# Performance work log

Measured on AMD Instinct MI355X. Metric: run time of the kernel, lower is better.

## Reference

```python
import jax, jax.numpy as jnp
import numpy as np

B, S, D, H = 2, 2048, 1024, 16
HD = D // H            # head_dim = 64
CHUNK = 1024           # hard-coded in the torch module
ROPE_THETA = 10000.0


def setup_inputs() -> dict:
    key = jax.random.key(0)
    ks = jax.random.split(key, 5)
    hidden_states = jax.random.normal(ks[0], (B, S, D), dtype=jnp.float32)
    # Precomputed RoPE frequencies: freqs_cis[s, j] = exp(i * s * theta_j),
    # stored as real [S, HD//2, 2] = (cos, sin).
    inv_freq = 1.0 / (ROPE_THETA ** (np.arange(0, HD, 2, dtype=np.float32) / HD))
    ang = np.outer(np.arange(S, dtype=np.float32), inv_freq)  # [S, HD//2]
    freqs_cis = jnp.stack([jnp.cos(ang), jnp.sin(ang)], axis=-1).astype(jnp.float32)
    scale = 0.02
    Wq = jax.random.normal(ks[1], (D, D), dtype=jnp.float32) * scale
    Wk = jax.random.normal(ks[2], (D, D), dtype=jnp.float32) * scale
    Wv = jax.random.normal(ks[3], (D, D), dtype=jnp.float32) * scale
    Wo = jax.random.normal(ks[4], (D, D), dtype=jnp.float32) * scale
    return {"hidden_states": hidden_states, "freqs_cis": freqs_cis,
            "Wq": Wq, "Wk": Wk, "Wv": Wv, "Wo": Wo}


def _apply_rope(x, freqs_cis):
    # x: [B, S, H, HD]; freqs_cis: [S, HD//2, 2] (cos, sin)
    b, s, h, hd = x.shape
    xr = x.reshape(b, s, h, hd // 2, 2)
    a, bb = xr[..., 0], xr[..., 1]
    c = freqs_cis[:s, :, 0][None, :, None, :]  # broadcast over batch, heads
    d = freqs_cis[:s, :, 1][None, :, None, :]
    # complex multiply (a + ib)(c + id)
    out = jnp.stack([a * c - bb * d, a * d + bb * c], axis=-1)
    return out.reshape(b, s, h, hd)


def reference(hidden_states, freqs_cis, Wq, Wk, Wv, Wo):
    b, s, dm = hidden_states.shape
    q = (hidden_states @ Wq).reshape(b, s, H, HD)
    k = (hidden_states @ Wk).reshape(b, s, H, HD)
    v = (hidden_states @ Wv).reshape(b, s, H, HD)
    q = _apply_rope(q, freqs_cis)
    k = _apply_rope(k, freqs_cis)
    q = q.transpose(0, 2, 1, 3)  # [B, H, S, HD]
    k = k.transpose(0, 2, 1, 3)
    v = v.transpose(0, 2, 1, 3)
    scaling = HD ** (-0.5)
    out = jnp.zeros_like(q)
    # Faithful replication of the (buggy) chunked attention: softmax is
    # normalized PER key-chunk, then chunk outputs are summed.
    for i in range(0, s, CHUNK):
        j = min(i + CHUNK, s)
        w = jnp.einsum('bhqd,bhkd->bhqk', q, k[:, :, i:j]) * scaling
        w = jax.nn.softmax(w.astype(jnp.float32), axis=-1).astype(q.dtype)
        out = out + jnp.einsum('bhqk,bhkd->bhqd', w, v[:, :, i:j])
    out = out.transpose(0, 2, 1, 3).reshape(b, s, dm)
    return out @ Wo
```

## Files before the change

kernel.cpp:

```cpp
#include <hip/hip_runtime.h>
#include <hip/hip_bf16.h>
#include <cstdint>

typedef __bf16 bf16x8 __attribute__((ext_vector_type(8)));
typedef float f32x4 __attribute__((ext_vector_type(4)));
typedef float f32x16 __attribute__((ext_vector_type(16)));

#define MFMA16(a, b, c) __builtin_amdgcn_mfma_f32_16x16x32_bf16(a, b, c, 0, 0, 0)
#define MFMA32(a, b, c) __builtin_amdgcn_mfma_f32_32x32x16_bf16(a, b, c, 0, 0, 0)

__device__ __forceinline__ void gload_lds16(const void* g, void* l) {
  __builtin_amdgcn_global_load_lds(
      (const __attribute__((address_space(1))) unsigned int*)g,
      (__attribute__((address_space(3))) unsigned int*)l, 16, 0, 0);
}

__device__ __forceinline__ unsigned short f2bf(float x) {
  union { float f; uint32_t u; } v; v.f = x;
  uint32_t r = v.u + 0x7fff + ((v.u >> 16) & 1);
  return (unsigned short)(r >> 16);
}
__device__ __forceinline__ float bf2f(unsigned short h) {
  union { float f; uint32_t u; } v; v.u = ((uint32_t)h) << 16;
  return v.f;
}
__device__ __forceinline__ f32x16 fzero16() {
  f32x16 v;
#pragma unroll
  for (int i = 0; i < 16; ++i) v[i] = 0.f;
  return v;
}

__global__ __launch_bounds__(256) void k_split(const float* __restrict__ x,
                                               unsigned short* __restrict__ hi, int n4) {
  int i = blockIdx.x * blockDim.x + threadIdx.x;
  if (i >= n4) return;
  float4 v = ((const float4*)x)[i];
  ushort4 h;
  h.x = f2bf(v.x); h.y = f2bf(v.y); h.z = f2bf(v.z); h.w = f2bf(v.w);
  ((ushort4*)hi)[i] = h;
}

__global__ __launch_bounds__(256) void k_wsplit(
    const float* __restrict__ Wq, const float* __restrict__ Wk,
    const float* __restrict__ Wv, const float* __restrict__ Wo,
    unsigned short* __restrict__ WtqH, unsigned short* __restrict__ WtkH,
    unsigned short* __restrict__ WtvH, unsigned short* __restrict__ WtoH) {
  const int z = blockIdx.z;
  const float* W = (z == 0) ? Wq : (z == 1) ? Wk : (z == 2) ? Wv : Wo;
  unsigned short* WtH = (z == 0) ? WtqH : (z == 1) ? WtkH : (z == 2) ? WtvH : WtoH;
  __shared__ float tile[32][33];
  const int bx = blockIdx.x, by = blockIdx.y;
  const int tx = threadIdx.x & 31, ty = threadIdx.x >> 5;
#pragma unroll
  for (int i = 0; i < 4; ++i)
    tile[ty + i * 8][tx] = W[(size_t)(by * 32 + ty + i * 8) * 1024 + bx * 32 + tx];
  __syncthreads();
#pragma unroll
  for (int i = 0; i < 4; ++i) {
    float v = tile[tx][ty + i * 8];
    WtH[(size_t)(bx * 32 + ty + i * 8) * 1024 + by * 32 + tx] = f2bf(v);
  }
}

__global__ __launch_bounds__(256, 2) void k_qkv(
    const unsigned short* __restrict__ hsH,
    const unsigned short* __restrict__ WqH, const unsigned short* __restrict__ WkH,
    const unsigned short* __restrict__ WvH, const float* __restrict__ freqs,
    unsigned short* __restrict__ qB, unsigned short* __restrict__ kB,
    unsigned short* __restrict__ vB) {
  __shared__ unsigned short Ah[128 * 32], Bh[128 * 32];
  const int tid = threadIdx.x;
  const int bm = blockIdx.y, bn = blockIdx.x;
  const int w = bn >> 3;
  const int n0 = (bn & 7) * 128;
  const unsigned short* WH = (w == 0) ? WqH : (w == 1) ? WkH : WvH;
  const int lane = tid & 63, wave = tid >> 6;
  const int wm = (wave & 1) * 64, wn = (wave >> 1) * 64;
  const int l15 = lane & 15, lq = lane >> 4;

  f32x4 acc[4][4];
#pragma unroll
  for (int i = 0; i < 4; i++)
#pragma unroll
    for (int j = 0; j < 4; j++) acc[i][j] = (f32x4){0.f, 0.f, 0.f, 0.f};

  const char* baseA = (const char*)hsH + (size_t)(bm * 128) * 2048;
  const char* baseB = (const char*)WH + (size_t)n0 * 2048;
  const int off0 = tid << 4, row0 = off0 >> 6, seg0 = off0 & 63;
  const int off1 = (tid + 256) << 4, row1 = off1 >> 6, seg1 = off1 & 63;

  for (int k0 = 0; k0 < 1024; k0 += 32) {
    __syncthreads();
    gload_lds16(baseA + (size_t)row0 * 2048 + k0 * 2 + seg0, (char*)Ah + wave * 1024);
    gload_lds16(baseB + (size_t)row0 * 2048 + k0 * 2 + seg0, (char*)Bh + wave * 1024);
    gload_lds16(baseA + (size_t)row1 * 2048 + k0 * 2 + seg1,
                (char*)Ah + 4096 + wave * 1024);
    gload_lds16(baseB + (size_t)row1 * 2048 + k0 * 2 + seg1,
                (char*)Bh + 4096 + wave * 1024);
    __syncthreads();
    bf16x8 ah[4], bh[4];
#pragma unroll
    for (int i = 0; i < 4; ++i) {
      ah[i] = *(const bf16x8*)&Ah[(wm + i * 16 + l15) * 32 + lq * 8];
      bh[i] = *(const bf16x8*)&Bh[(wn + i * 16 + l15) * 32 + lq * 8];
    }
#pragma unroll
    for (int i = 0; i < 4; ++i)
#pragma unroll
      for (int j = 0; j < 4; ++j) acc[i][j] = MFMA16(ah[i], bh[j], acc[i][j]);
  }

  unsigned short* dst = (w == 0) ? qB : (w == 1) ? kB : vB;
#pragma unroll
  for (int i = 0; i < 4; ++i) {
#pragma unroll
    for (int j = 0; j < 4; ++j) {
      int colw = n0 + wn + j * 16 + l15;
      int h = colw >> 6, d = colw & 63;
#pragma unroll
      for (int r = 0; r < 4; ++r) {
        int rowg = bm * 128 + wm + i * 16 + lq * 4 + r;
        int s = rowg & 2047, b = rowg >> 11;
        float val = acc[i][j][r];
        if (w < 2) {
          float partner = __shfl_xor(val, 1);
          int jj = d >> 1;
          float cs = freqs[(s * 32 + jj) * 2 + 0];
          float sn = freqs[(s * 32 + jj) * 2 + 1];
          float res = (d & 1) ? (partner * sn + val * cs) : (val * cs - partner * sn);
          dst[(((size_t)(b * 16 + h)) * 2048 + s) * 64 + d] = f2bf(res);
        } else {
          dst[(((size_t)(b * 16 + h)) * 64 + d) * 2048 + s] = f2bf(val);
        }
      }
    }
  }
}

#define LDP 72

__global__ __launch_bounds__(256, 2) void k_attn(
    const unsigned short* __restrict__ qB, const unsigned short* __restrict__ kB,
    const unsigned short* __restrict__ vB,
    unsigned short* __restrict__ c0, unsigned short* __restrict__ c1) {
  __shared__ unsigned short Pt[4 * 64 * LDP];
  const int tid = threadIdx.x, lane = tid & 63, wave = tid >> 6;
  const int l31 = lane & 31, lh = lane >> 5;
  const int bid = blockIdx.x;
  const int x = (bid >> 3) & 7;
  const int gg = (bid & 7) + 8 * (bid >> 6);
  const int bh = gg & 31;
  const int chunk = gg >> 5;
  const int q0 = x * 256 + wave * 64;
  const size_t base = (size_t)bh * 2048 * 64;
  const float sc = 0.125f * 1.44269504089f;

  bf16x8 qf[2][4];
#pragma unroll
  for (int qt = 0; qt < 2; ++qt)
#pragma unroll
    for (int ks = 0; ks < 4; ++ks)
      qf[qt][ks] = *(const bf16x8*)(qB + base + (size_t)(q0 + qt * 32 + l31) * 64 +
                                    ks * 16 + lh * 8);

  const unsigned short* kp = kB + base + (size_t)chunk * 1024 * 64 + l31 * 64 + lh * 8;
  const unsigned short* vp = vB + base + l31 * 2048 + chunk * 1024 + lh * 8;
  unsigned short* Pw = Pt + wave * (64 * LDP);

  bf16x8 kfa[4], kfb[4];
#pragma unroll
  for (int ks = 0; ks < 4; ++ks) {
    kfa[ks] = *(const bf16x8*)(kp + ks * 16);
    kfb[ks] = *(const bf16x8*)(kp + 2048 + ks * 16);
  }
  kp += 4096;

  f32x16 o[2][2];
#pragma unroll
  for (int a = 0; a < 2; ++a)
#pragma unroll
    for (int bq = 0; bq < 2; ++bq) o[a][bq] = fzero16();
  float rsum[2] = {0.f, 0.f};

  for (int kb = 0; kb < 16; ++kb) {
    bf16x8 vf[2][4];
#pragma unroll
    for (int dt = 0; dt < 2; ++dt)
#pragma unroll
      for (int ks = 0; ks < 4; ++ks)
        vf[dt][ks] = *(const bf16x8*)(vp + dt * 65536 + ks * 16);

#pragma unroll
    for (int mt = 0; mt < 2; ++mt) {
      f32x16 s0 = fzero16(), s1 = fzero16();
      if (mt == 0) {
#pragma unroll
        for (int ks = 0; ks < 4; ++ks) {
          s0 = MFMA32(kfa[ks], qf[0][ks], s0);
          s1 = MFMA32(kfa[ks], qf[1][ks], s1);
        }
#pragma unroll
        for (int ks = 0; ks < 4; ++ks) kfa[ks] = *(const bf16x8*)(kp + ks * 16);
      } else {
#pragma unroll
        for (int ks = 0; ks < 4; ++ks) {
          s0 = MFMA32(kfb[ks], qf[0][ks], s0);
          s1 = MFMA32(kfb[ks], qf[1][ks], s1);
        }
#pragma unroll
        for (int ks = 0; ks < 4; ++ks)
          kfb[ks] = *(const bf16x8*)(kp + 2048 + ks * 16);
      }
#pragma unroll
      for (int qt = 0; qt < 2; ++qt) {
        const f32x16& sv = qt ? s1 : s0;
        float ps[16];
        float rs = 0.f;
#pragma unroll
        for (int r = 0; r < 16; ++r) {
          ps[r] = __builtin_exp2f(sv[r] * sc);
          rs += ps[r];
        }
        rsum[qt] += rs;
        unsigned int* prow =
            (unsigned int*)(Pw + (qt * 32 + l31) * LDP + mt * 32 + 4 * lh);
#pragma unroll
        for (int p = 0; p < 8; ++p) {
          union { unsigned int u; __bf16 h2[2]; } pk;
          pk.h2[0] = (__bf16)ps[2 * p];
          pk.h2[1] = (__bf16)ps[2 * p + 1];
          prow[4 * (p >> 1) + (p & 1)] = pk.u;
        }
      }
    }
    kp += 4096;

#pragma unroll
    for (int qt = 0; qt < 2; ++qt)
#pragma unroll
      for (int ks = 0; ks < 4; ++ks) {
        bf16x8 pf = *(const bf16x8*)(Pw + (qt * 32 + l31) * LDP + ks * 16 + lh * 8);
        o[0][qt] = MFMA32(vf[0][ks], pf, o[0][qt]);
        o[1][qt] = MFMA32(vf[1][ks], pf, o[1][qt]);
      }
    vp += 64;
  }

  unsigned short* cB = chunk ? c1 : c0;
  const int b = bh >> 4, h = bh & 15;
#pragma unroll
  for (int qt = 0; qt < 2; ++qt) {
    float lsum = rsum[qt] + __shfl_xor(rsum[qt], 32);
    float inv = 1.f / lsum;
    int s = q0 + qt * 32 + l31;
#pragma unroll
    for (int dt = 0; dt < 2; ++dt)
#pragma unroll
      for (int g = 0; g < 4; ++g) {
        int d = dt * 32 + 4 * lh + 8 * g;
        size_t idx = ((size_t)(b * 2048 + s)) * 1024 + h * 64 + d;
        ushort4 hv;
#pragma unroll
        for (int t = 0; t < 4; ++t)
          ((unsigned short*)&hv)[t] = f2bf(o[dt][qt][g * 4 + t] * inv);
        *(ushort4*)(cB + idx) = hv;
      }
  }
}

__global__ __launch_bounds__(256) void k_comb(const unsigned short* __restrict__ c0,
                                              const unsigned short* __restrict__ c1,
                                              unsigned short* __restrict__ outB,
                                              int n8) {
  int i = blockIdx.x * blockDim.x + threadIdx.x;
  if (i >= n8) return;
  uint4 a = ((const uint4*)c0)[i];
  uint4 b = ((const uint4*)c1)[i];
  uint4 r;
  const unsigned short* pa = (const unsigned short*)&a;
  const unsigned short* pb = (const unsigned short*)&b;
  unsigned short* pr = (unsigned short*)&r;
#pragma unroll
  for (int j = 0; j < 8; ++j) pr[j] = f2bf(bf2f(pa[j]) + bf2f(pb[j]));
  ((uint4*)outB)[i] = r;
}

__global__ __launch_bounds__(256, 2) void k_out(const unsigned short* __restrict__ A,
                                                const unsigned short* __restrict__ B,
                                                float* __restrict__ out) {
  __shared__ unsigned short Ah[128 * 32], Bh[128 * 32];
  const int tid = threadIdx.x;
  const int bm = blockIdx.y, n0 = blockIdx.x * 128;
  const int lane = tid & 63, wave = tid >> 6;
  const int wm = (wave & 1) * 64, wn = (wave >> 1) * 64;
  const int l15 = lane & 15, lq = lane >> 4;

  f32x4 acc[4][4];
#pragma unroll
  for (int i = 0; i < 4; i++)
#pragma unroll
    for (int j = 0; j < 4; j++) acc[i][j] = (f32x4){0.f, 0.f, 0.f, 0.f};

  const char* baseA = (const char*)A + (size_t)(bm * 128) * 2048;
  const char* baseB = (const char*)B + (size_t)n0 * 2048;
  const int off0 = tid << 4, row0 = off0 >> 6, seg0 = off0 & 63;
  const int off1 = (tid + 256) << 4, row1 = off1 >> 6, seg1 = off1 & 63;

  for (int k0 = 0; k0 < 1024; k0 += 32) {
    __syncthreads();
    gload_lds16(baseA + (size_t)row0 * 2048 + k0 * 2 + seg0, (char*)Ah + wave * 1024);
    gload_lds16(baseB + (size_t)row0 * 2048 + k0 * 2 + seg0, (char*)Bh + wave * 1024);
    gload_lds16(baseA + (size_t)row1 * 2048 + k0 * 2 + seg1,
                (char*)Ah + 4096 + wave * 1024);
    gload_lds16(baseB + (size_t)row1 * 2048 + k0 * 2 + seg1,
                (char*)Bh + 4096 + wave * 1024);
    __syncthreads();
    bf16x8 ah[4], bh[4];
#pragma unroll
    for (int i = 0; i < 4; ++i) {
      ah[i] = *(const bf16x8*)&Ah[(wm + i * 16 + l15) * 32 + lq * 8];
      bh[i] = *(const bf16x8*)&Bh[(wn + i * 16 + l15) * 32 + lq * 8];
    }
#pragma unroll
    for (int i = 0; i < 4; ++i)
#pragma unroll
      for (int j = 0; j < 4; ++j) acc[i][j] = MFMA16(ah[i], bh[j], acc[i][j]);
  }
#pragma unroll
  for (int i = 0; i < 4; ++i)
#pragma unroll
    for (int j = 0; j < 4; ++j) {
      int colw = n0 + wn + j * 16 + l15;
#pragma unroll
      for (int r = 0; r < 4; ++r) {
        int rowg = bm * 128 + wm + i * 16 + lq * 4 + r;
        out[(size_t)rowg * 1024 + colw] = acc[i][j][r];
      }
    }
}

extern "C" void kernel_launch(void* const* d_in, const int* in_sizes, int n_in,
                              void* d_out, int out_size, void* d_ws, size_t ws_size,
                              hipStream_t stream) {
  const float* hs = (const float*)d_in[0];
  const float* freqs = (const float*)d_in[1];
  const float* Wq = (const float*)d_in[2];
  const float* Wk = (const float*)d_in[3];
  const float* Wv = (const float*)d_in[4];
  const float* Wo = (const float*)d_in[5];
  float* out = (float*)d_out;

  const size_t MD = (size_t)4096 * 1024;
  const size_t WW = (size_t)1024 * 1024;
  unsigned short* hsH = (unsigned short*)d_ws;
  unsigned short* WtqH = hsH + MD;
  unsigned short* WtkH = WtqH + WW;
  unsigned short* WtvH = WtkH + WW;
  unsigned short* WtoH = WtvH + WW;
  unsigned short* qB = WtoH + WW;
  unsigned short* kB = qB + MD;
  unsigned short* vB = kB + MD;
  unsigned short* c0 = vB + MD;
  unsigned short* c1 = c0 + MD;
  unsigned short* attnB = hsH;

  k_split<<<4096, 256, 0, stream>>>(hs, hsH, (int)(MD / 4));
  k_wsplit<<<dim3(32, 32, 4), 256, 0, stream>>>(Wq, Wk, Wv, Wo,
                                                WtqH, WtkH, WtvH, WtoH);
  k_qkv<<<dim3(24, 32), 256, 0, stream>>>(hsH, WtqH, WtkH, WtvH, freqs, qB, kB, vB);
  k_attn<<<512, 256, 0, stream>>>(qB, kB, vB, c0, c1);
  k_comb<<<2048, 256, 0, stream>>>(c0, c1, attnB, (int)(MD / 8));
  k_out<<<dim3(8, 32), 256, 0, stream>>>(attnB, WtoH, out);
}
```

Before: 258.7 us.

## Split attention keys into four partial chunks and unroll QKV GEMM K-loop

```diff
diff --git a/kernel.cpp b/kernel.cpp
--- a/kernel.cpp
+++ b/kernel.cpp
@@ -69,7 +69,8 @@
     const unsigned short* __restrict__ WvH, const float* __restrict__ freqs,
     unsigned short* __restrict__ qB, unsigned short* __restrict__ kB,
     unsigned short* __restrict__ vB) {
-  __shared__ unsigned short Ah[128 * 32], Bh[128 * 32];
+  __shared__ unsigned short Ah0[128 * 32], Bh0[128 * 32];
+  __shared__ unsigned short Ah1[128 * 32], Bh1[128 * 32];
   const int tid = threadIdx.x;
   const int bm = blockIdx.y, bn = blockIdx.x;
   const int w = bn >> 3;
@@ -90,20 +91,37 @@
   const int off0 = tid << 4, row0 = off0 >> 6, seg0 = off0 & 63;
   const int off1 = (tid + 256) << 4, row1 = off1 >> 6, seg1 = off1 & 63;
 
-  for (int k0 = 0; k0 < 1024; k0 += 32) {
+  for (int k0 = 0; k0 < 1024; k0 += 64) {
     __syncthreads();
-    gload_lds16(baseA + (size_t)row0 * 2048 + k0 * 2 + seg0, (char*)Ah + wave * 1024);
-    gload_lds16(baseB + (size_t)row0 * 2048 + k0 * 2 + seg0, (char*)Bh + wave * 1024);
+    gload_lds16(baseA + (size_t)row0 * 2048 + k0 * 2 + seg0, (char*)Ah0 + wave * 1024);
+    gload_lds16(baseB + (size_t)row0 * 2048 + k0 * 2 + seg0, (char*)Bh0 + wave * 1024);
     gload_lds16(baseA + (size_t)row1 * 2048 + k0 * 2 + seg1,
-                (char*)Ah + 4096 + wave * 1024);
+                (char*)Ah0 + 4096 + wave * 1024);
     gload_lds16(baseB + (size_t)row1 * 2048 + k0 * 2 + seg1,
-                (char*)Bh + 4096 + wave * 1024);
+                (char*)Bh0 + 4096 + wave * 1024);
+    gload_lds16(baseA + (size_t)row0 * 2048 + (k0 + 32) * 2 + seg0,
+                (char*)Ah1 + wave * 1024);
+    gload_lds16(baseB + (size_t)row0 * 2048 + (k0 + 32) * 2 + seg0,
+                (char*)Bh1 + wave * 1024);
+    gload_lds16(baseA + (size_t)row1 * 2048 + (k0 + 32) * 2 + seg1,
+                (char*)Ah1 + 4096 + wave * 1024);
+    gload_lds16(baseB + (size_t)row1 * 2048 + (k0 + 32) * 2 + seg1,
+                (char*)Bh1 + 4096 + wave * 1024);
     __syncthreads();
     bf16x8 ah[4], bh[4];
 #pragma unroll
     for (int i = 0; i < 4; ++i) {
-      ah[i] = *(const bf16x8*)&Ah[(wm + i * 16 + l15) * 32 + lq * 8];
-      bh[i] = *(const bf16x8*)&Bh[(wn + i * 16 + l15) * 32 + lq * 8];
+      ah[i] = *(const bf16x8*)&Ah0[(wm + i * 16 + l15) * 32 + lq * 8];
+      bh[i] = *(const bf16x8*)&Bh0[(wn + i * 16 + l15) * 32 + lq * 8];
+    }
+#pragma unroll
+    for (int i = 0; i < 4; ++i)
+#pragma unroll
+      for (int j = 0; j < 4; ++j) acc[i][j] = MFMA16(ah[i], bh[j], acc[i][j]);
+#pragma unroll
+    for (int i = 0; i < 4; ++i) {
+      ah[i] = *(const bf16x8*)&Ah1[(wm + i * 16 + l15) * 32 + lq * 8];
+      bh[i] = *(const bf16x8*)&Bh1[(wn + i * 16 + l15) * 32 + lq * 8];
     }
 #pragma unroll
     for (int i = 0; i < 4; ++i)
@@ -140,10 +158,10 @@
 
 #define LDP 72
 
-__global__ __launch_bounds__(256, 2) void k_attn(
+__global__ __launch_bounds__(256, 3) void k_attn(
     const unsigned short* __restrict__ qB, const unsigned short* __restrict__ kB,
     const unsigned short* __restrict__ vB,
-    unsigned short* __restrict__ c0, unsigned short* __restrict__ c1) {
+    unsigned short* __restrict__ cP, float* __restrict__ rsW) {
   __shared__ unsigned short Pt[4 * 64 * LDP];
   const int tid = threadIdx.x, lane = tid & 63, wave = tid >> 6;
   const int l31 = lane & 31, lh = lane >> 5;
@@ -151,7 +169,8 @@
   const int x = (bid >> 3) & 7;
   const int gg = (bid & 7) + 8 * (bid >> 6);
   const int bh = gg & 31;
-  const int chunk = gg >> 5;
+  const int z = gg >> 5;
+  const int key00 = (z >> 1) * 1024 + (z & 1) * 512;
   const int q0 = x * 256 + wave * 64;
   const size_t base = (size_t)bh * 2048 * 64;
   const float sc = 0.125f * 1.44269504089f;
@@ -164,8 +183,8 @@
       qf[qt][ks] = *(const bf16x8*)(qB + base + (size_t)(q0 + qt * 32 + l31) * 64 +
                                     ks * 16 + lh * 8);
 
-  const unsigned short* kp = kB + base + (size_t)chunk * 1024 * 64 + l31 * 64 + lh * 8;
-  const unsigned short* vp = vB + base + l31 * 2048 + chunk * 1024 + lh * 8;
+  const unsigned short* kp = kB + base + (size_t)key00 * 64 + l31 * 64 + lh * 8;
+  const unsigned short* vp = vB + base + l31 * 2048 + key00 + lh * 8;
   unsigned short* Pw = Pt + wave * (64 * LDP);
 
   bf16x8 kfa[4], kfb[4];
@@ -183,7 +202,7 @@
     for (int bq = 0; bq < 2; ++bq) o[a][bq] = fzero16();
   float rsum[2] = {0.f, 0.f};
 
-  for (int kb = 0; kb < 16; ++kb) {
+  for (int kb = 0; kb < 8; ++kb) {
     bf16x8 vf[2][4];
 #pragma unroll
     for (int dt = 0; dt < 2; ++dt)
@@ -247,13 +266,13 @@
     vp += 64;
   }
 
-  unsigned short* cB = chunk ? c1 : c0;
+  unsigned short* cB = cP + (size_t)z * (4096 * 1024);
   const int b = bh >> 4, h = bh & 15;
 #pragma unroll
   for (int qt = 0; qt < 2; ++qt) {
     float lsum = rsum[qt] + __shfl_xor(rsum[qt], 32);
-    float inv = 1.f / lsum;
     int s = q0 + qt * 32 + l31;
+    if (lh == 0) rsW[((size_t)z * 32 + bh) * 2048 + s] = lsum;
 #pragma unroll
     for (int dt = 0; dt < 2; ++dt)
 #pragma unroll
@@ -263,26 +282,43 @@
         ushort4 hv;
 #pragma unroll
         for (int t = 0; t < 4; ++t)
-          ((unsigned short*)&hv)[t] = f2bf(o[dt][qt][g * 4 + t] * inv);
+          ((unsigned short*)&hv)[t] = f2bf(o[dt][qt][g * 4 + t]);
         *(ushort4*)(cB + idx) = hv;
       }
   }
 }
 
-__global__ __launch_bounds__(256) void k_comb(const unsigned short* __restrict__ c0,
-                                              const unsigned short* __restrict__ c1,
+__global__ __launch_bounds__(256) void k_comb(const unsigned short* __restrict__ cP,
+                                              const float* __restrict__ rsW,
                                               unsigned short* __restrict__ outB,
                                               int n8) {
   int i = blockIdx.x * blockDim.x + threadIdx.x;
   if (i >= n8) return;
-  uint4 a = ((const uint4*)c0)[i];
-  uint4 b = ((const uint4*)c1)[i];
+  const size_t MD = (size_t)4096 * 1024;
+  int flat = i * 8;
+  int col = flat & 1023;
+  int srow = (flat >> 10) & 2047;
+  int b = flat >> 21;
+  int bh = b * 16 + (col >> 6);
+  float l0 = rsW[(size_t)(0 * 32 + bh) * 2048 + srow] +
+             rsW[(size_t)(1 * 32 + bh) * 2048 + srow];
+  float l1 = rsW[(size_t)(2 * 32 + bh) * 2048 + srow] +
+             rsW[(size_t)(3 * 32 + bh) * 2048 + srow];
+  float i0 = 1.f / l0, i1 = 1.f / l1;
+  uint4 a0 = ((const uint4*)cP)[i];
+  uint4 a1 = ((const uint4*)(cP + MD))[i];
+  uint4 a2 = ((const uint4*)(cP + 2 * MD))[i];
+  uint4 a3 = ((const uint4*)(cP + 3 * MD))[i];
   uint4 r;
-  const unsigned short* pa = (const unsigned short*)&a;
-  const unsigned short* pb = (const unsigned short*)&b;
+  const unsigned short* p0 = (const unsigned short*)&a0;
+  const unsigned short* p1 = (const unsigned short*)&a1;
+  const unsigned short* p2 = (const unsigned short*)&a2;
+  const unsigned short* p3 = (const unsigned short*)&a3;
   unsigned short* pr = (unsigned short*)&r;
 #pragma unroll
-  for (int j = 0; j < 8; ++j) pr[j] = f2bf(bf2f(pa[j]) + bf2f(pb[j]));
+  for (int j = 0; j < 8; ++j)
+    pr[j] = f2bf((bf2f(p0[j]) + bf2f(p1[j])) * i0 +
+                 (bf2f(p2[j]) + bf2f(p3[j])) * i1);
   ((uint4*)outB)[i] = r;
 }
 
@@ -361,15 +397,15 @@
   unsigned short* qB = WtoH + WW;
   unsigned short* kB = qB + MD;
   unsigned short* vB = kB + MD;
-  unsigned short* c0 = vB + MD;
-  unsigned short* c1 = c0 + MD;
+  unsigned short* cP = vB + MD;
+  float* rsW = (float*)(cP + 4 * MD);
   unsigned short* attnB = hsH;
 
   k_split<<<4096, 256, 0, stream>>>(hs, hsH, (int)(MD / 4));
   k_wsplit<<<dim3(32, 32, 4), 256, 0, stream>>>(Wq, Wk, Wv, Wo,
                                                 WtqH, WtkH, WtvH, WtoH);
   k_qkv<<<dim3(24, 32), 256, 0, stream>>>(hsH, WtqH, WtkH, WtvH, freqs, qB, kB, vB);
-  k_attn<<<512, 256, 0, stream>>>(qB, kB, vB, c0, c1);
-  k_comb<<<2048, 256, 0, stream>>>(c0, c1, attnB, (int)(MD / 8));
+  k_attn<<<1024, 256, 0, stream>>>(qB, kB, vB, cP, rsW);
+  k_comb<<<2048, 256, 0, stream>>>(cP, rsW, attnB, (int)(MD / 8));
   k_out<<<dim3(8, 32), 256, 0, stream>>>(attnB, WtoH, out);
 }
```

Result: slower. 329.3 us (+27.3%).
